# Kernel tuning notes

Measured on AMD Instinct MI355X. Metric: run time of the kernel, lower is better.

Reference implementation:

```python
import jax, jax.numpy as jnp
import numpy as np

B, H, W = 2, 512, 512
EPS = 1e-7


def conv2d(x, w, b, stride=1, pad=1):
    y = jax.lax.conv_general_dilated(x, w, (stride, stride), [(pad, pad), (pad, pad)],
                                     dimension_numbers=('NCHW', 'OIHW', 'NCHW'))
    return y + b[None, :, None, None]


def prelu(x, a):
    return jnp.where(x >= 0, x, a * x)


def feature_ext(x, ws, bs, aa):
    # three-level pyramid: 32ch@full, 64ch@1/2, 96ch@1/4
    x = prelu(conv2d(x, ws[0], bs[0]), aa[0])
    fea1 = prelu(conv2d(x, ws[1], bs[1]), aa[1])
    x = prelu(conv2d(fea1, ws[2], bs[2], stride=2), aa[2])
    fea2 = prelu(conv2d(x, ws[3], bs[3]), aa[3])
    x = prelu(conv2d(fea2, ws[4], bs[4], stride=2), aa[4])
    fea3 = prelu(conv2d(x, ws[5], bs[5]), aa[5])
    return fea1, fea2, fea3


def backwarp(x, flow):
    # grid_sample(bilinear, padding_mode='border', align_corners=True) with pixel-space flow
    b, c, h, w = x.shape
    gy, gx = jnp.meshgrid(jnp.arange(h, dtype=x.dtype), jnp.arange(w, dtype=x.dtype), indexing='ij')
    px = jnp.clip(gx[None] + flow[:, 0], 0.0, w - 1.0)  # (B,h,w)
    py = jnp.clip(gy[None] + flow[:, 1], 0.0, h - 1.0)
    x0f = jnp.floor(px); y0f = jnp.floor(py)
    wx = px - x0f; wy = py - y0f
    x0 = x0f.astype(jnp.int32); y0 = y0f.astype(jnp.int32)
    x1 = jnp.minimum(x0 + 1, w - 1); y1 = jnp.minimum(y0 + 1, h - 1)
    xf = x.reshape(b, c, h * w)

    def gather(ix, iy):
        idx = (iy * w + ix).reshape(b, -1)
        return jax.vmap(lambda v, i: v[:, i])(xf, idx).reshape(b, c, h, w)

    return (gather(x0, y0) * ((1 - wx) * (1 - wy))[:, None]
            + gather(x1, y0) * (wx * (1 - wy))[:, None]
            + gather(x0, y1) * ((1 - wx) * wy)[:, None]
            + gather(x1, y1) * (wx * wy)[:, None])


def softsplat(ten, flow, z):
    # softmax splatting: scatter-add of exp(z)-weighted values + exp(z) normalizer
    b, c, h, w = ten.shape
    ez = jnp.exp(z)                                      # (B,1,h,w)
    vals = jnp.concatenate([ten * ez, ez], axis=1)       # (B,C+1,h,w)
    gy, gx = jnp.meshgrid(jnp.arange(h, dtype=ten.dtype), jnp.arange(w, dtype=ten.dtype), indexing='ij')
    fx = gx[None] + flow[:, 0]
    fy = gy[None] + flow[:, 1]
    x0f = jnp.floor(fx); y0f = jnp.floor(fy)
    x0 = x0f.astype(jnp.int32); y0 = y0f.astype(jnp.int32)
    x1 = x0 + 1; y1 = y0 + 1
    wx1 = fx - x0f; wy1 = fy - y0f
    wx0 = 1.0 - wx1; wy0 = 1.0 - wy1
    corners = [(x0, y0, wx0 * wy0), (x1, y0, wx1 * wy0), (x0, y1, wx0 * wy1), (x1, y1, wx1 * wy1)]
    idxs, wts = [], []
    for cx, cy, cw in corners:
        valid = (cx >= 0) & (cx < w) & (cy >= 0) & (cy < h)
        idxs.append(jnp.where(valid, cy * w + cx, 0).reshape(b, -1))
        wts.append(jnp.where(valid, cw, 0.0).reshape(b, -1))
    idx = jnp.stack(idxs, 1)  # (B,4,HW)
    wt = jnp.stack(wts, 1)
    vflat = vals.reshape(b, c + 1, h * w)

    def scat(v, i, ww):  # v (C+1,HW), i (4,HW), ww (4,HW)
        contrib = (v[:, None, :] * ww[None]).reshape(c + 1, -1)
        return jnp.zeros((c + 1, h * w), v.dtype).at[:, i.reshape(-1)].add(contrib)

    out = jax.vmap(scat)(vflat, idx, wt).reshape(b, c + 1, h, w)
    return out[:, :c] / (out[:, c:] + EPS)


def resize_bl(x, out_h, out_w):
    # bilinear resize, align_corners=False (half-pixel), matches torch interpolate on downsample
    b, c, h, w = x.shape

    def coords(n_out, n_in):
        pos = jnp.clip((jnp.arange(n_out, dtype=x.dtype) + 0.5) * (n_in / n_out) - 0.5, 0.0, n_in - 1.0)
        p0 = jnp.floor(pos)
        i0 = p0.astype(jnp.int32)
        i1 = jnp.minimum(i0 + 1, n_in - 1)
        return i0, i1, pos - p0

    iy0, iy1, wy = coords(out_h, h)
    ix0, ix1, wx = coords(out_w, w)
    x = x[:, :, iy0] * (1 - wy)[None, None, :, None] + x[:, :, iy1] * wy[None, None, :, None]
    x = x[:, :, :, ix0] * (1 - wx) + x[:, :, :, ix1] * wx
    return x


def _forward(input_0, input_1, target_t, flows01, flows10, ws, bs, aa, param_scale):
    fea0 = feature_ext(input_0, ws, bs, aa)
    fea1 = feature_ext(input_1, ws, bs, aa)
    t = target_t[:, None, None, None]

    def splat_map(i0, i1, flows, feas, tt):
        p0 = i0 * 2 - 1
        p1 = i1 * 2 - 1
        err = jnp.mean(jnp.abs(p0 - backwarp(p1, flows[0])), axis=1, keepdims=True)
        z = param_scale * jax.lax.stop_gradient(err)
        imgs, feats = [], []
        for s in range(3):
            f = tt * flows[s]
            hh, ww = H >> s, W >> s
            img = i0 if s == 0 else resize_bl(i0, hh, ww)
            zz = z if s == 0 else resize_bl(z, hh, ww)
            flow_t0 = softsplat(-f, f, zz)
            imgs.append(backwarp(img, flow_t0))
            feats.append(backwarp(feas[s], flow_t0))
        return imgs, feats

    wi0, wf0 = splat_map(input_0, input_1, flows01, fea0, t)
    wi1, wf1 = splat_map(input_1, input_0, flows10, fea1, 1.0 - t)
    level0 = jnp.concatenate([wi0[0], wf0[0], wi1[0], wf1[0]], axis=1)  # (B,70,H,W)
    level1 = jnp.concatenate([wf0[1], wf1[1]], axis=1)                  # (B,128,H/2,W/2)
    level2 = jnp.concatenate([wf0[2], wf1[2]], axis=1)                  # (B,192,H/4,W/4)
    return level0, level1, level2


def setup_inputs() -> dict:
    key = jax.random.key(0)
    ks = jax.random.split(key, 24)
    d = {}
    d['input_0'] = jax.random.uniform(ks[0], (B, 3, H, W), jnp.float32)
    d['input_1'] = jax.random.uniform(ks[1], (B, 3, H, W), jnp.float32)
    d['target_t'] = jax.random.uniform(ks[2], (B,), jnp.float32)
    for i, (nm, s) in enumerate([('flow01_0', 0), ('flow01_1', 1), ('flow01_2', 2),
                                 ('flow10_0', 0), ('flow10_1', 1), ('flow10_2', 2)]):
        d[nm] = jax.random.normal(ks[3 + i], (B, 2, H >> s, W >> s), jnp.float32) * (8.0 / (2 ** s))
    shapes = [(32, 3), (32, 32), (64, 32), (64, 64), (96, 64), (96, 96)]
    for i, (o, c) in enumerate(shapes):
        d['w%d' % (i + 1)] = jax.random.normal(ks[9 + i], (o, c, 3, 3), jnp.float32) * 0.05
        d['b%d' % (i + 1)] = jnp.zeros((o,), jnp.float32)
    d['prelu_a'] = jnp.full((6,), 0.25, jnp.float32)
    d['param_scale'] = jnp.full((1, 1, 1, 1), -1.0, jnp.float32)
    return d


def reference(input_0, input_1, target_t, flow01_0, flow01_1, flow01_2,
              flow10_0, flow10_1, flow10_2,
              w1, b1, w2, b2, w3, b3, w4, b4, w5, b5, w6, b6, prelu_a, param_scale):
    ws = [w1, w2, w3, w4, w5, w6]
    bs = [b1, b2, b3, b4, b5, b6]
    aa = [prelu_a[i] for i in range(6)]
    return _forward(input_0, input_1, target_t,
                    [flow01_0, flow01_1, flow01_2],
                    [flow10_0, flow10_1, flow10_2], ws, bs, aa, param_scale)
```

## Files before the change

kernel.cpp:

```cpp
#include <hip/hip_runtime.h>
#include <math.h>

#define EPSF 1e-7f
constexpr int BB = 2, HH = 512, WWC = 512;

typedef __attribute__((ext_vector_type(4))) float f32x4;
typedef __attribute__((ext_vector_type(8))) _Float16 half8;

struct HZ {
    _Float16* p;
    int Hp, Wp, C;
};
struct HZ5 {
    HZ e[5];
};
__global__ void halo_zero_kernel(HZ5 z) {
    HZ d = z.e[blockIdx.y];
    const int wc = d.Wp * d.C;
    const int side = (d.Hp - 2) * d.C;
    const int perB = 2 * wc + 2 * side;
    const int total = 4 * perB;
    for (int i = blockIdx.x * 256 + threadIdx.x; i < total;
         i += gridDim.x * 256) {
        int b = i / perB, r = i % perB;
        int y, x, c;
        if (r < wc) {
            y = 0; x = r / d.C; c = r % d.C;
        } else if (r < 2 * wc) {
            int q = r - wc;
            y = d.Hp - 1; x = q / d.C; c = q % d.C;
        } else {
            int q = r - 2 * wc;
            int sd = q / side, q2 = q % side;
            y = 1 + q2 / d.C; x = sd ? d.Wp - 1 : 0; c = q2 % d.C;
        }
        d.p[(((size_t)b * d.Hp + y) * d.Wp + x) * d.C + c] = (_Float16)0.f;
    }
}

struct WL {
    const float* w;
    _Float16* dst;
    int IC, OC;
};
struct WL5 {
    WL e[5];
};
__global__ void weight_swz_kernel(WL5 wl) {
    WL d = wl.e[blockIdx.y];
    const int IC = d.IC;
    const int K9 = 9 * IC;
    const int NKC = K9 / 32;
    const int total = d.OC * K9;
    for (int i = blockIdx.x * 256 + threadIdx.x; i < total;
         i += gridDim.x * 256) {
        int j = i & 7;
        int lane = (i >> 3) & 63;
        int rest = i >> 9;
        int kc = rest % NKC;
        int fo = rest / NKC;
        int f = fo & 1, ocblk = fo >> 1;
        int l15 = lane & 15, g = lane >> 4;
        int k = kc * 32 + g * 8 + j;
        int pos = k / IC, ic = k % IC;
        int oc = ocblk * 32 + f * 16 + l15;
        d.dst[i] = (_Float16)d.w[((size_t)oc * IC + ic) * 9 + pos];
    }
}

template <int OCT, int YT>
__global__ __launch_bounds__(256) void conv3x3_nhwc(
    const float* __restrict__ in0, const float* __restrict__ in1,
    const float* __restrict__ wgt, const float* __restrict__ bias,
    const float* __restrict__ prelu_a, int aidx, _Float16* __restrict__ out,
    int IC, int OC, int IH, int IW, int OWp) {
    const int OH = IH, OW = IW;
    extern __shared__ float wsh[];
    const int oc0 = blockIdx.z * OCT;
    const int nw = OCT * IC * 9;
    const float* wsrc = wgt + (size_t)oc0 * IC * 9;
    for (int i = threadIdx.y * 64 + threadIdx.x; i < nw; i += 256)
        wsh[i] = wsrc[i];
    __syncthreads();

    const int ox = blockIdx.x * 64 + threadIdx.x;
    const int BROWS = 4 * YT;
    const int tiles_y = OH / BROWS;
    const int oy0 = (blockIdx.y % tiles_y) * BROWS + threadIdx.y * YT;
    const int b = blockIdx.y / tiles_y;

    float acc[OCT][YT];
#pragma unroll
    for (int j = 0; j < OCT; j++) {
        float bj = bias[oc0 + j];
#pragma unroll
        for (int yy = 0; yy < YT; yy++) acc[j][yy] = bj;
    }

    constexpr int R = YT + 2;
    const float* inb = (b < 2 ? in0 : in1) + (size_t)(b & 1) * IC * IH * IW;
    const int iy0 = oy0 - 1, ix0 = ox - 1;

    for (int ic = 0; ic < IC; ic++) {
        const float* ip = inb + (size_t)ic * IH * IW;
        float v[R][3];
#pragma unroll
        for (int r = 0; r < R; r++) {
            const int iy = iy0 + r;
            const bool yok = (unsigned)iy < (unsigned)IH;
            const float* rp = ip + iy * IW;
#pragma unroll
            for (int c = 0; c < 3; c++) {
                const int ix = ix0 + c;
                v[r][c] = (yok && (unsigned)ix < (unsigned)IW) ? rp[ix] : 0.f;
            }
        }
#pragma unroll
        for (int j = 0; j < OCT; j++) {
            const float* wj = wsh + (j * IC + ic) * 9;
            float w[9];
#pragma unroll
            for (int k = 0; k < 9; k++) w[k] = wj[k];
#pragma unroll
            for (int yy = 0; yy < YT; yy++) {
                float a = acc[j][yy];
#pragma unroll
                for (int ky = 0; ky < 3; ky++)
#pragma unroll
                    for (int kx = 0; kx < 3; kx++)
                        a = fmaf(v[yy + ky][kx], w[ky * 3 + kx], a);
                acc[j][yy] = a;
            }
        }
    }
    const float al = prelu_a[aidx];
    const int OHp = OH + 2;
#pragma unroll
    for (int yy = 0; yy < YT; yy++) {
        _Float16* ob =
            out + (((size_t)b * OHp + (oy0 + yy + 1)) * OWp + (ox + 1)) * OC;
#pragma unroll
        for (int j = 0; j < OCT; j++) {
            float y = acc[j][yy];
            y = y >= 0.f ? y : al * y;
            ob[oc0 + j] = (_Float16)y;
        }
    }
}

template <int S, int IC, int ROWS>
__global__ __launch_bounds__(256) void conv_mfma2(
    const _Float16* __restrict__ in, const _Float16* __restrict__ wswz,
    const float* __restrict__ bias, const float* __restrict__ prelu_a,
    int aidx, _Float16* __restrict__ out, int OC, int IWp, int OH, int OW,
    int OWp) {
    constexpr int NICC = IC / 32;
    constexpr int NKC = 9 * NICC;
    constexpr int NSTG = 2 * NKC * 512;
    extern __shared__ _Float16 bsh[];
    const int oc0 = blockIdx.z * 32;
    {
        const _Float16* src = wswz + (size_t)blockIdx.z * NSTG;
        for (int i = threadIdx.x * 8; i < NSTG; i += 256 * 8)
            *(half8*)(bsh + i) = *(const half8*)(src + i);
    }
    __syncthreads();

    const int lane = threadIdx.x & 63, w = threadIdx.x >> 6;
    const int l15 = lane & 15, g = lane >> 4;
    const int ny = OH / ROWS;
    const int oy0 = (blockIdx.y % ny) * ROWS;
    const int b = blockIdx.y / ny;
    const int xb = blockIdx.x * 128 + w * 32;
    const int IHp = OH * S + 2;
    const _Float16* inb = in + (size_t)b * IHp * IWp * IC;
    const float bv0 = bias[oc0 + l15], bv1 = bias[oc0 + 16 + l15];
    const float al = prelu_a[aidx];
    const size_t aoff0 = (size_t)(xb + l15) * S * IC + g * 8;
    const size_t aoff1 = aoff0 + (size_t)16 * S * IC;
    _Float16* outb = out + (size_t)b * (OH + 2) * OWp * OC;

    for (int ry = 0; ry < ROWS; ++ry) {
        const int oy = oy0 + ry;
        f32x4 acc00 = {bv0, bv0, bv0, bv0}, acc01 = {bv1, bv1, bv1, bv1};
        f32x4 acc10 = {bv0, bv0, bv0, bv0}, acc11 = {bv1, bv1, bv1, bv1};
#pragma unroll
        for (int pos = 0; pos < 9; ++pos) {
            const int ky = pos / 3, kx = pos % 3;
            const _Float16* ap =
                inb + ((size_t)(oy * S + ky) * IWp + kx) * IC;
#pragma unroll
            for (int icc = 0; icc < NICC; ++icc) {
                const int kc = pos * NICC + icc;
                half8 a0 = *(const half8*)(ap + aoff0 + icc * 32);
                half8 a1 = *(const half8*)(ap + aoff1 + icc * 32);
                half8 b0 = *(const half8*)(bsh + kc * 512 + lane * 8);
                half8 b1 = *(const half8*)(bsh + (NKC + kc) * 512 + lane * 8);
                acc00 = __builtin_amdgcn_mfma_f32_16x16x32_f16(a0, b0, acc00,
                                                               0, 0, 0);
                acc01 = __builtin_amdgcn_mfma_f32_16x16x32_f16(a0, b1, acc01,
                                                               0, 0, 0);
                acc10 = __builtin_amdgcn_mfma_f32_16x16x32_f16(a1, b0, acc10,
                                                               0, 0, 0);
                acc11 = __builtin_amdgcn_mfma_f32_16x16x32_f16(a1, b1, acc11,
                                                               0, 0, 0);
            }
        }
#define STORE_FRAG(A, M, N)                                                   \
    {                                                                         \
        _Pragma("unroll") for (int r = 0; r < 4; ++r) {                       \
            int x = xb + (M)*16 + g * 4 + r;                                  \
            float v = (A)[r];                                                 \
            v = v >= 0.f ? v : al * v;                                        \
            outb[((size_t)(oy + 1) * OWp + (x + 1)) * OC + oc0 + (N)*16 +     \
                 l15] = (_Float16)v;                                          \
        }                                                                     \
    }
        STORE_FRAG(acc00, 0, 0)
        STORE_FRAG(acc01, 0, 1)
        STORE_FRAG(acc10, 1, 0)
        STORE_FRAG(acc11, 1, 1)
#undef STORE_FRAG
    }
}

__global__ void compute_z2_kernel(const float* __restrict__ in0,
                                  const float* __restrict__ in1,
                                  const float* __restrict__ f01,
                                  const float* __restrict__ f10,
                                  const float* __restrict__ pscale,
                                  float* __restrict__ z0,
                                  float* __restrict__ z1) {
    int idx = blockIdx.x * blockDim.x + threadIdx.x;
    const int n = BB * HH * WWC;
    if (idx >= n) return;
    const int dir = blockIdx.y;
    const float* i0 = dir ? in1 : in0;
    const float* i1 = dir ? in0 : in1;
    const float* flow = dir ? f10 : f01;
    float* z = dir ? z1 : z0;
    int x = idx % WWC, y = (idx / WWC) % HH, b = idx / (WWC * HH);
    const float* fb = flow + (size_t)b * 2 * HH * WWC;
    float fx = fb[y * WWC + x];
    float fy = fb[HH * WWC + y * WWC + x];
    float px = fminf(fmaxf(x + fx, 0.f), WWC - 1.f);
    float py = fminf(fmaxf(y + fy, 0.f), HH - 1.f);
    float x0f = floorf(px), y0f = floorf(py);
    int x0 = (int)x0f, y0 = (int)y0f;
    int x1 = min(x0 + 1, WWC - 1), y1 = min(y0 + 1, HH - 1);
    float wx = px - x0f, wy = py - y0f;
    float w00 = (1.f - wx) * (1.f - wy), w10 = wx * (1.f - wy);
    float w01 = (1.f - wx) * wy, w11 = wx * wy;
    const float* ib0 = i0 + (size_t)b * 3 * HH * WWC;
    const float* ib1 = i1 + (size_t)b * 3 * HH * WWC;
    float err = 0.f;
#pragma unroll
    for (int c = 0; c < 3; c++) {
        const float* sp = ib1 + (size_t)c * HH * WWC;
        float wv = sp[y0 * WWC + x0] * w00 + sp[y0 * WWC + x1] * w10 +
                   sp[y1 * WWC + x0] * w01 + sp[y1 * WWC + x1] * w11;
        float p0 = 2.f * ib0[(size_t)c * HH * WWC + y * WWC + x] - 1.f;
        err += fabsf(p0 - (2.f * wv - 1.f));
    }
    z[idx] = pscale[0] * (err * (1.f / 3.f));
}

__device__ inline void atomic_add_f32(float* p, float v) {
    __hip_atomic_fetch_add(p, v, __ATOMIC_RELAXED, __HIP_MEMORY_SCOPE_AGENT);
}

__device__ inline float z_sample(const float* __restrict__ zb, int b, int sx,
                                 int sy, int s) {
    const float* zp = zb + (size_t)b * HH * WWC;
    if (s == 0) return zp[sy * WWC + sx];
    float sc = (float)(1 << s);
    float px = fminf(fmaxf((sx + 0.5f) * sc - 0.5f, 0.f), WWC - 1.f);
    float py = fminf(fmaxf((sy + 0.5f) * sc - 0.5f, 0.f), HH - 1.f);
    float x0f = floorf(px), y0f = floorf(py);
    int x0 = (int)x0f, y0 = (int)y0f;
    int x1 = min(x0 + 1, WWC - 1), y1 = min(y0 + 1, HH - 1);
    float wx = px - x0f, wy = py - y0f;
    return zp[y0 * WWC + x0] * (1.f - wx) * (1.f - wy) +
           zp[y0 * WWC + x1] * wx * (1.f - wy) +
           zp[y1 * WWC + x0] * (1.f - wx) * wy + zp[y1 * WWC + x1] * wx * wy;
}

__global__ void splat_far_kernel(const float* __restrict__ fl0,
                                 const float* __restrict__ fl1,
                                 const float* __restrict__ z0,
                                 const float* __restrict__ z1,
                                 const float* __restrict__ tptr,
                                 float* __restrict__ acc, int s, int hh,
                                 int ww) {
    int idx = blockIdx.x * blockDim.x + threadIdx.x;
    const int n = BB * hh * ww;
    if (idx >= n) return;
    const int dir = blockIdx.y;
    const float* flow = dir ? fl1 : fl0;
    const float* z = dir ? z1 : z0;
    float* accd = acc + (size_t)dir * BB * 3 * hh * ww;
    int x = idx % ww, y = (idx / ww) % hh, b = idx / (ww * hh);
    float tt = tptr[b];
    if (dir) tt = 1.f - tt;
    const float* fb = flow + (size_t)b * 2 * hh * ww;
    float fx = tt * fb[y * ww + x];
    float fy = tt * fb[hh * ww + y * ww + x];
    if (fmaxf(fabsf(fx), fabsf(fy)) <= 15.f) return;
    float zz = z_sample(z, b, x, y, s);
    float ez = expf(zz);
    float vx = -fx * ez, vy = -fy * ez;
    float tx = x + fx, ty = y + fy;
    float x0f = floorf(tx), y0f = floorf(ty);
    int x0 = (int)x0f, y0 = (int)y0f;
    int x1 = x0 + 1, y1 = y0 + 1;
    float wx1 = tx - x0f, wy1 = ty - y0f;
    float wx0 = 1.f - wx1, wy0 = 1.f - wy1;
    float* ab = accd + (size_t)b * 3 * hh * ww;
    int cxs[4] = {x0, x1, x0, x1};
    int cys[4] = {y0, y0, y1, y1};
    float cws[4] = {wx0 * wy0, wx1 * wy0, wx0 * wy1, wx1 * wy1};
#pragma unroll
    for (int k = 0; k < 4; k++) {
        int cx = cxs[k], cy = cys[k];
        float w = cws[k];
        if (cx >= 0 && cx < ww && cy >= 0 && cy < hh && w != 0.f) {
            float* p = ab + (size_t)3 * (cy * ww + cx);
            atomic_add_f32(p, vx * w);
            atomic_add_f32(p + 1, vy * w);
            atomic_add_f32(p + 2, ez * w);
        }
    }
}

template <int TH, int TW>
__global__ __launch_bounds__(256) void splat_gather_kernel(
    const float* __restrict__ fl0, const float* __restrict__ fl1,
    const float* __restrict__ z0, const float* __restrict__ z1,
    const float* __restrict__ tptr, float* __restrict__ acc, int s, int hh,
    int ww) {
    constexpr int HALO = 16;
    constexpr int RH = TH + 2 * HALO, RW = TW + 2 * HALO;
    __shared__ float lacc[TH * TW * 3];
    const int x0 = blockIdx.x * TW, y0 = blockIdx.y * TH;
    const int comp = blockIdx.z;
    const int b = comp & (BB - 1), dir = comp / BB;
    const float* flow = dir ? fl1 : fl0;
    const float* z = dir ? z1 : z0;
    float* accd = acc + (size_t)dir * BB * 3 * hh * ww;
    const int tid = threadIdx.x;
    for (int i = tid; i < TH * TW * 3; i += 256) lacc[i] = 0.f;
    __syncthreads();
    float tt = tptr[b];
    if (dir) tt = 1.f - tt;
    const float* fb = flow + (size_t)b * 2 * hh * ww;
    for (int i = tid; i < RH * RW; i += 256) {
        int sy = y0 - HALO + i / RW;
        int sx = x0 - HALO + i % RW;
        if ((unsigned)sy >= (unsigned)hh || (unsigned)sx >= (unsigned)ww)
            continue;
        float fx = tt * fb[sy * ww + sx];
        float fy = tt * fb[(size_t)hh * ww + sy * ww + sx];
        if (fmaxf(fabsf(fx), fabsf(fy)) > 15.f) continue;
        float zz = z_sample(z, b, sx, sy, s);
        float ez = expf(zz);
        float vx = -fx * ez, vy = -fy * ez;
        float tx = sx + fx, ty = sy + fy;
        float xf = floorf(tx), yf = floorf(ty);
        int cx0 = (int)xf - x0, cy0 = (int)yf - y0;
        float wx1 = tx - xf, wy1 = ty - yf;
        float wx0 = 1.f - wx1, wy0 = 1.f - wy1;
#pragma unroll
        for (int k = 0; k < 4; k++) {
            int cx = cx0 + (k & 1), cy = cy0 + (k >> 1);
            float wgt = ((k & 1) ? wx1 : wx0) * ((k >> 1) ? wy1 : wy0);
            if ((unsigned)cx < (unsigned)TW && (unsigned)cy < (unsigned)TH &&
                wgt != 0.f) {
                float* p = lacc + (cy * TW + cx) * 3;
                atomicAdd(p, vx * wgt);
                atomicAdd(p + 1, vy * wgt);
                atomicAdd(p + 2, ez * wgt);
            }
        }
    }
    __syncthreads();
    float* ab = accd + (((size_t)b * hh + y0) * ww + x0) * 3;
    for (int i = tid; i < TH * TW * 3; i += 256) {
        int row = i / (TW * 3), rem = i % (TW * 3);
        float* gp = ab + (size_t)row * ww * 3 + rem;
        *gp = *gp + lacc[i];
    }
}

__global__ void backwarp_s0_kernel(const float* __restrict__ acc,
                                   const float* __restrict__ in0,
                                   const float* __restrict__ in1,
                                   const _Float16* __restrict__ f1,
                                   float* __restrict__ out) {
    int idx = blockIdx.x * blockDim.x + threadIdx.x;
    const int plane = HH * WWC;
    const int n = BB * plane;
    if (idx >= n) return;
    const int dir = blockIdx.y;
    int x = idx % WWC, y = (idx / WWC) % HH, b = idx / plane;
    const float* accd = acc + (size_t)dir * BB * 3 * plane;
    int o = y * WWC + x;
    const float* ap = accd + ((size_t)b * plane + o) * 3;
    float den = ap[2] + EPSF;
    float fx = ap[0] / den;
    float fy = ap[1] / den;
    float px = fminf(fmaxf(x + fx, 0.f), WWC - 1.f);
    float py = fminf(fmaxf(y + fy, 0.f), HH - 1.f);
    float x0f = floorf(px), y0f = floorf(py);
    int x0 = (int)x0f, y0 = (int)y0f;
    int x1 = min(x0 + 1, WWC - 1), y1 = min(y0 + 1, HH - 1);
    float wx = px - x0f, wy = py - y0f;
    float w00 = (1.f - wx) * (1.f - wy), w10 = wx * (1.f - wy);
    float w01 = (1.f - wx) * wy, w11 = wx * wy;
    float* ob = out + (((size_t)b * 70 + dir * 35) * (size_t)plane) + o;
    {
        const float* sb = (dir ? in1 : in0) + (size_t)b * 3 * plane;
        int i00 = y0 * WWC + x0, i10 = y0 * WWC + x1, i01 = y1 * WWC + x0,
            i11 = y1 * WWC + x1;
#pragma unroll
        for (int c = 0; c < 3; c++) {
            const float* sp = sb + (size_t)c * plane;
            float v = sp[i00] * w00 + sp[i10] * w10 + sp[i01] * w01 +
                      sp[i11] * w11;
            ob[(size_t)c * plane] = v;
        }
    }
    {
        const int Wp = WWC + 2, C = 32;
        const _Float16* sb = f1 + (size_t)(dir * 2 + b) * (HH + 2) * Wp * C;
        const _Float16* s00 = sb + ((size_t)(y0 + 1) * Wp + x0 + 1) * C;
        const _Float16* s10 = sb + ((size_t)(y0 + 1) * Wp + x1 + 1) * C;
        const _Float16* s01 = sb + ((size_t)(y1 + 1) * Wp + x0 + 1) * C;
        const _Float16* s11 = sb + ((size_t)(y1 + 1) * Wp + x1 + 1) * C;
        float* obf = ob + (size_t)3 * plane;
        for (int c8 = 0; c8 < C; c8 += 8) {
            half8 v00 = *(const half8*)(s00 + c8);
            half8 v10 = *(const half8*)(s10 + c8);
            half8 v01 = *(const half8*)(s01 + c8);
            half8 v11 = *(const half8*)(s11 + c8);
#pragma unroll
            for (int k = 0; k < 8; k++) {
                float v = (float)v00[k] * w00 + (float)v10[k] * w10 +
                          (float)v01[k] * w01 + (float)v11[k] * w11;
                obf[(size_t)(c8 + k) * plane] = v;
            }
        }
    }
}

__global__ void backwarp_feat_kernel(const float* __restrict__ acc,
                                     const _Float16* __restrict__ src,
                                     float* __restrict__ out, int C, int hh,
                                     int ww, int Wp) {
    int idx = blockIdx.x * blockDim.x + threadIdx.x;
    const int n = BB * hh * ww;
    if (idx >= n) return;
    const int dir = blockIdx.y;
    int x = idx % ww, y = (idx / ww) % hh, b = idx / (ww * hh);
    const int plane = hh * ww;
    const float* accd = acc + (size_t)dir * BB * 3 * plane;
    const float* ap = accd + ((size_t)b * plane + y * ww + x) * 3;
    float den = ap[2] + EPSF;
    float fx = ap[0] / den;
    float fy = ap[1] / den;
    float px = fminf(fmaxf(x + fx, 0.f), ww - 1.f);
    float py = fminf(fmaxf(y + fy, 0.f), hh - 1.f);
    float x0f = floorf(px), y0f = floorf(py);
    int x0 = (int)x0f, y0 = (int)y0f;
    int x1 = min(x0 + 1, ww - 1), y1 = min(y0 + 1, hh - 1);
    float wx = px - x0f, wy = py - y0f;
    float w00 = (1.f - wx) * (1.f - wy), w10 = wx * (1.f - wy);
    float w01 = (1.f - wx) * wy, w11 = wx * wy;
    const int Hp = hh + 2;
    const _Float16* sb = src + (size_t)(dir * 2 + b) * Hp * Wp * C;
    const _Float16* s00 = sb + ((size_t)(y0 + 1) * Wp + x0 + 1) * C;
    const _Float16* s10 = sb + ((size_t)(y0 + 1) * Wp + x1 + 1) * C;
    const _Float16* s01 = sb + ((size_t)(y1 + 1) * Wp + x0 + 1) * C;
    const _Float16* s11 = sb + ((size_t)(y1 + 1) * Wp + x1 + 1) * C;
    float* ob = out + (((size_t)b * 2 * C + dir * C) * (size_t)plane) +
                y * ww + x;
    for (int c8 = 0; c8 < C; c8 += 8) {
        half8 v00 = *(const half8*)(s00 + c8);
        half8 v10 = *(const half8*)(s10 + c8);
        half8 v01 = *(const half8*)(s01 + c8);
        half8 v11 = *(const half8*)(s11 + c8);
#pragma unroll
        for (int k = 0; k < 8; k++) {
            float v = (float)v00[k] * w00 + (float)v10[k] * w10 +
                      (float)v01[k] * w01 + (float)v11[k] * w11;
            ob[(size_t)(c8 + k) * plane] = v;
        }
    }
}

extern "C" void kernel_launch(void* const* d_in, const int* in_sizes, int n_in,
                              void* d_out, int out_size, void* d_ws,
                              size_t ws_size, hipStream_t stream) {
    const float* input0 = (const float*)d_in[0];
    const float* input1 = (const float*)d_in[1];
    const float* tgt = (const float*)d_in[2];
    const float* flows[2][3] = {
        {(const float*)d_in[3], (const float*)d_in[4], (const float*)d_in[5]},
        {(const float*)d_in[6], (const float*)d_in[7], (const float*)d_in[8]}};
    const float* w[6];
    const float* bs[6];
    for (int i = 0; i < 6; i++) {
        w[i] = (const float*)d_in[9 + 2 * i];
        bs[i] = (const float*)d_in[10 + 2 * i];
    }
    const float* prelu_a = (const float*)d_in[21];
    const float* pscale = (const float*)d_in[22];
    float* out = (float*)d_out;

    _Float16* hb = (_Float16*)d_ws;
    const size_t A1 = (size_t)4 * 514 * 514 * 32;
    const size_t A2 = (size_t)4 * 258 * 258 * 64;
    const size_t A3 = (size_t)4 * 130 * 130 * 96;
    _Float16* act1 = hb;
    _Float16* f1 = act1 + A1;
    _Float16* act2 = f1 + A1;
    _Float16* f2 = act2 + A2;
    _Float16* act3 = f2 + A2;
    _Float16* f3 = act3 + A3;
    float* fb32 = (float*)(f3 + A3);
    float* zb0 = fb32;
    float* zb1 = zb0 + (size_t)BB * HH * WWC;
    float* acc = zb1 + (size_t)BB * HH * WWC;
    _Float16* wswz = (_Float16*)(acc + (size_t)2 * BB * 3 * HH * WWC);
    const size_t WO2 = 0, WO3 = 9216, WO4 = 27648, WO5 = 64512, WO6 = 119808;

    {
        WL5 wlist;
        wlist.e[0] = {w[1], wswz + WO2, 32, 32};
        wlist.e[1] = {w[2], wswz + WO3, 32, 64};
        wlist.e[2] = {w[3], wswz + WO4, 64, 64};
        wlist.e[3] = {w[4], wswz + WO5, 64, 96};
        wlist.e[4] = {w[5], wswz + WO6, 96, 96};
        dim3 grd(16, 5);
        weight_swz_kernel<<<grd, 256, 0, stream>>>(wlist);
    }
    {
        HZ5 hz;
        hz.e[0] = {act1, 514, 514, 32};
        hz.e[1] = {f1, 514, 514, 32};
        hz.e[2] = {act2, 258, 258, 64};
        hz.e[3] = {f2, 258, 258, 64};
        hz.e[4] = {act3, 130, 130, 96};
        dim3 grd(32, 5);
        halo_zero_kernel<<<grd, 256, 0, stream>>>(hz);
    }

    {
        dim3 blk(64, 4);
        dim3 grd(512 / 64, (512 / 16) * 4, 32 / 16);
        size_t sm = (size_t)16 * 3 * 9 * sizeof(float);
        conv3x3_nhwc<16, 4><<<grd, blk, sm, stream>>>(
            input0, input1, w[0], bs[0], prelu_a, 0, act1, 3, 32, 512, 512,
            514);
    }
    {
        dim3 grd(512 / 128, (512 / 4) * 4, 1);
        conv_mfma2<1, 32, 4><<<grd, 256, 18432, stream>>>(
            act1, wswz + WO2, bs[1], prelu_a, 1, f1, 32, 514, 512, 512, 514);
    }
    {
        dim3 grd(256 / 128, (256 / 4) * 4, 2);
        conv_mfma2<2, 32, 4><<<grd, 256, 18432, stream>>>(
            f1, wswz + WO3, bs[2], prelu_a, 2, act2, 64, 514, 256, 256, 258);
    }
    {
        dim3 grd(256 / 128, (256 / 4) * 4, 2);
        conv_mfma2<1, 64, 4><<<grd, 256, 36864, stream>>>(
            act2, wswz + WO4, bs[3], prelu_a, 3, f2, 64, 258, 256, 256, 258);
    }
    {
        dim3 grd(1, (128 / 2) * 4, 3);
        conv_mfma2<2, 64, 2><<<grd, 256, 36864, stream>>>(
            f2, wswz + WO5, bs[4], prelu_a, 4, act3, 96, 258, 128, 128, 130);
    }
    {
        dim3 grd(1, (128 / 2) * 4, 3);
        conv_mfma2<1, 96, 2><<<grd, 256, 55296, stream>>>(
            act3, wswz + WO6, bs[5], prelu_a, 5, f3, 96, 130, 128, 128, 130);
    }

    {
        int n = BB * HH * WWC;
        dim3 grd((n + 255) / 256, 2);
        compute_z2_kernel<<<grd, 256, 0, stream>>>(
            input0, input1, flows[0][0], flows[1][0], pscale, zb0, zb1);
    }

    const size_t l1off = (size_t)BB * 70 * 512 * 512;
    const size_t l2off = l1off + (size_t)BB * 128 * 256 * 256;

    for (int s = 0; s < 3; s++) {
        int hh = HH >> s, ww = WWC >> s;
        int n = BB * hh * ww;
        hipMemsetAsync(acc, 0, (size_t)2 * BB * 3 * hh * ww * sizeof(float),
                       stream);
        {
            dim3 grd((n + 255) / 256, 2);
            splat_far_kernel<<<grd, 256, 0, stream>>>(
                flows[0][s], flows[1][s], zb0, zb1, tgt, acc, s, hh, ww);
        }
        if (s < 2) {
            dim3 grd(ww / 64, hh / 32, 2 * BB);
            splat_gather_kernel<32, 64><<<grd, 256, 0, stream>>>(
                flows[0][s], flows[1][s], zb0, zb1, tgt, acc, s, hh, ww);
        } else {
            dim3 grd(ww / 32, hh / 16, 2 * BB);
            splat_gather_kernel<16, 32><<<grd, 256, 0, stream>>>(
                flows[0][s], flows[1][s], zb0, zb1, tgt, acc, s, hh, ww);
        }
        dim3 grd((n + 255) / 256, 2);
        if (s == 0) {
            backwarp_s0_kernel<<<grd, 256, 0, stream>>>(acc, input0, input1,
                                                        f1, out);
        } else if (s == 1) {
            backwarp_feat_kernel<<<grd, 256, 0, stream>>>(
                acc, f2, out + l1off, 64, 256, 256, 258);
        } else {
            backwarp_feat_kernel<<<grd, 256, 0, stream>>>(
                acc, f3, out + l2off, 96, 128, 128, 130);
        }
    }
}
```

Before: 1.000 ms.

## Restructure MFMA conv to compute all output channels per wave, read weights from global

The MFMA conv kernel is rewritten so each wave computes a 64-pixel strip across all output channels (4 M-fragments by OC/16 N-fragments) instead of 32 pixels by 32 channels. Input activations are then loaded once per pixel for every output channel rather than once per 32-channel block. Weight staging through shared memory is removed, and B fragments are read directly from global memory, relying on cache. The weight swizzle layout is flattened to match. The cost is more accumulator registers per thread, possibly lower occupancy, and weight reads that no longer come from LDS.

```diff
diff --git a/kernel.cpp b/kernel.cpp
--- a/kernel.cpp
+++ b/kernel.cpp
@@ -58,12 +58,11 @@
         int lane = (i >> 3) & 63;
         int rest = i >> 9;
         int kc = rest % NKC;
-        int fo = rest / NKC;
-        int f = fo & 1, ocblk = fo >> 1;
+        int N = rest / NKC;
         int l15 = lane & 15, g = lane >> 4;
         int k = kc * 32 + g * 8 + j;
         int pos = k / IC, ic = k % IC;
-        int oc = ocblk * 32 + f * 16 + l15;
+        int oc = N * 16 + l15;
         d.dst[i] = (_Float16)d.w[((size_t)oc * IC + ic) * 9 + pos];
     }
 }
@@ -148,80 +147,74 @@
     }
 }
 
-template <int S, int IC, int ROWS>
-__global__ __launch_bounds__(256) void conv_mfma2(
+template <int S, int IC, int OC, int WPR>
+__global__ __launch_bounds__(256) void conv_mfma3(
     const _Float16* __restrict__ in, const _Float16* __restrict__ wswz,
     const float* __restrict__ bias, const float* __restrict__ prelu_a,
-    int aidx, _Float16* __restrict__ out, int OC, int IWp, int OH, int OW,
-    int OWp) {
+    int aidx, _Float16* __restrict__ out, int IWp, int OH, int OW, int OWp) {
     constexpr int NICC = IC / 32;
     constexpr int NKC = 9 * NICC;
-    constexpr int NSTG = 2 * NKC * 512;
-    extern __shared__ _Float16 bsh[];
-    const int oc0 = blockIdx.z * 32;
-    {
-        const _Float16* src = wswz + (size_t)blockIdx.z * NSTG;
-        for (int i = threadIdx.x * 8; i < NSTG; i += 256 * 8)
-            *(half8*)(bsh + i) = *(const half8*)(src + i);
-    }
-    __syncthreads();
-
+    constexpr int NFR = OC / 16;
+    constexpr int RPB = 4 / WPR;
     const int lane = threadIdx.x & 63, w = threadIdx.x >> 6;
     const int l15 = lane & 15, g = lane >> 4;
-    const int ny = OH / ROWS;
-    const int oy0 = (blockIdx.y % ny) * ROWS;
+    const int ny = OH / RPB;
+    const int oy = (blockIdx.y % ny) * RPB + w / WPR;
     const int b = blockIdx.y / ny;
-    const int xb = blockIdx.x * 128 + w * 32;
+    const int xb = blockIdx.x * (WPR * 64) + (w % WPR) * 64;
     const int IHp = OH * S + 2;
     const _Float16* inb = in + (size_t)b * IHp * IWp * IC;
-    const float bv0 = bias[oc0 + l15], bv1 = bias[oc0 + 16 + l15];
     const float al = prelu_a[aidx];
-    const size_t aoff0 = (size_t)(xb + l15) * S * IC + g * 8;
-    const size_t aoff1 = aoff0 + (size_t)16 * S * IC;
+
+    f32x4 acc[4][NFR];
+#pragma unroll
+    for (int n = 0; n < NFR; ++n) {
+        float bv = bias[n * 16 + l15];
+#pragma unroll
+        for (int m = 0; m < 4; ++m) acc[m][n] = {bv, bv, bv, bv};
+    }
+    size_t aoff[4];
+#pragma unroll
+    for (int m = 0; m < 4; ++m)
+        aoff[m] = (size_t)(xb + m * 16 + l15) * S * IC + g * 8;
+    const int boff = lane * 8;
+
+#pragma unroll
+    for (int pos = 0; pos < 9; ++pos) {
+        const int ky = pos / 3, kx = pos % 3;
+        const _Float16* ap = inb + ((size_t)(oy * S + ky) * IWp + kx) * IC;
+#pragma unroll
+        for (int icc = 0; icc < NICC; ++icc) {
+            const int kc = pos * NICC + icc;
+            half8 a[4];
+#pragma unroll
+            for (int m = 0; m < 4; ++m)
+                a[m] = *(const half8*)(ap + aoff[m] + icc * 32);
+#pragma unroll
+            for (int n = 0; n < NFR; ++n) {
+                half8 bf = *(const half8*)(wswz +
+                                           (size_t)(n * NKC + kc) * 512 +
+                                           boff);
+#pragma unroll
+                for (int m = 0; m < 4; ++m)
+                    acc[m][n] = __builtin_amdgcn_mfma_f32_16x16x32_f16(
+                        a[m], bf, acc[m][n], 0, 0, 0);
+            }
+        }
+    }
     _Float16* outb = out + (size_t)b * (OH + 2) * OWp * OC;
-
-    for (int ry = 0; ry < ROWS; ++ry) {
-        const int oy = oy0 + ry;
-        f32x4 acc00 = {bv0, bv0, bv0, bv0}, acc01 = {bv1, bv1, bv1, bv1};
-        f32x4 acc10 = {bv0, bv0, bv0, bv0}, acc11 = {bv1, bv1, bv1, bv1};
-#pragma unroll
-        for (int pos = 0; pos < 9; ++pos) {
-            const int ky = pos / 3, kx = pos % 3;
-            const _Float16* ap =
-                inb + ((size_t)(oy * S + ky) * IWp + kx) * IC;
-#pragma unroll
-            for (int icc = 0; icc < NICC; ++icc) {
-                const int kc = pos * NICC + icc;
-                half8 a0 = *(const half8*)(ap + aoff0 + icc * 32);
-                half8 a1 = *(const half8*)(ap + aoff1 + icc * 32);
-                half8 b0 = *(const half8*)(bsh + kc * 512 + lane * 8);
-                half8 b1 = *(const half8*)(bsh + (NKC + kc) * 512 + lane * 8);
-                acc00 = __builtin_amdgcn_mfma_f32_16x16x32_f16(a0, b0, acc00,
-                                                               0, 0, 0);
-                acc01 = __builtin_amdgcn_mfma_f32_16x16x32_f16(a0, b1, acc01,
-                                                               0, 0, 0);
-                acc10 = __builtin_amdgcn_mfma_f32_16x16x32_f16(a1, b0, acc10,
-                                                               0, 0, 0);
-                acc11 = __builtin_amdgcn_mfma_f32_16x16x32_f16(a1, b1, acc11,
-                                                               0, 0, 0);
+#pragma unroll
+    for (int m = 0; m < 4; ++m)
+#pragma unroll
+        for (int n = 0; n < NFR; ++n)
+#pragma unroll
+            for (int r = 0; r < 4; ++r) {
+                int x = xb + m * 16 + g * 4 + r;
+                float v = acc[m][n][r];
+                v = v >= 0.f ? v : al * v;
+                outb[((size_t)(oy + 1) * OWp + (x + 1)) * OC + n * 16 + l15] =
+                    (_Float16)v;
             }
-        }
-#define STORE_FRAG(A, M, N)                                                   \
-    {                                                                         \
-        _Pragma("unroll") for (int r = 0; r < 4; ++r) {                       \
-            int x = xb + (M)*16 + g * 4 + r;                                  \
-            float v = (A)[r];                                                 \
-            v = v >= 0.f ? v : al * v;                                        \
-            outb[((size_t)(oy + 1) * OWp + (x + 1)) * OC + oc0 + (N)*16 +     \
-                 l15] = (_Float16)v;                                          \
-        }                                                                     \
-    }
-        STORE_FRAG(acc00, 0, 0)
-        STORE_FRAG(acc01, 0, 1)
-        STORE_FRAG(acc10, 1, 0)
-        STORE_FRAG(acc11, 1, 1)
-#undef STORE_FRAG
-    }
 }
 
 __global__ void compute_z2_kernel(const float* __restrict__ in0,
@@ -563,29 +556,29 @@
             514);
     }
     {
-        dim3 grd(512 / 128, (512 / 4) * 4, 1);
-        conv_mfma2<1, 32, 4><<<grd, 256, 18432, stream>>>(
-            act1, wswz + WO2, bs[1], prelu_a, 1, f1, 32, 514, 512, 512, 514);
-    }
-    {
-        dim3 grd(256 / 128, (256 / 4) * 4, 2);
-        conv_mfma2<2, 32, 4><<<grd, 256, 18432, stream>>>(
-            f1, wswz + WO3, bs[2], prelu_a, 2, act2, 64, 514, 256, 256, 258);
-    }
-    {
-        dim3 grd(256 / 128, (256 / 4) * 4, 2);
-        conv_mfma2<1, 64, 4><<<grd, 256, 36864, stream>>>(
-            act2, wswz + WO4, bs[3], prelu_a, 3, f2, 64, 258, 256, 256, 258);
-    }
-    {
-        dim3 grd(1, (128 / 2) * 4, 3);
-        conv_mfma2<2, 64, 2><<<grd, 256, 36864, stream>>>(
-            f2, wswz + WO5, bs[4], prelu_a, 4, act3, 96, 258, 128, 128, 130);
-    }
-    {
-        dim3 grd(1, (128 / 2) * 4, 3);
-        conv_mfma2<1, 96, 2><<<grd, 256, 55296, stream>>>(
-            act3, wswz + WO6, bs[5], prelu_a, 5, f3, 96, 130, 128, 128, 130);
+        dim3 grd(512 / 256, 512 * 4, 1);
+        conv_mfma3<1, 32, 32, 4><<<grd, 256, 0, stream>>>(
+            act1, wswz + WO2, bs[1], prelu_a, 1, f1, 514, 512, 512, 514);
+    }
+    {
+        dim3 grd(1, 256 * 4, 1);
+        conv_mfma3<2, 32, 64, 4><<<grd, 256, 0, stream>>>(
+            f1, wswz + WO3, bs[2], prelu_a, 2, act2, 514, 256, 256, 258);
+    }
+    {
+        dim3 grd(1, 256 * 4, 1);
+        conv_mfma3<1, 64, 64, 4><<<grd, 256, 0, stream>>>(
+            act2, wswz + WO4, bs[3], prelu_a, 3, f2, 258, 256, 256, 258);
+    }
+    {
+        dim3 grd(1, (128 / 2) * 4, 1);
+        conv_mfma3<2, 64, 96, 2><<<grd, 256, 0, stream>>>(
+            f2, wswz + WO5, bs[4], prelu_a, 4, act3, 258, 128, 128, 130);
+    }
+    {
+        dim3 grd(1, (128 / 2) * 4, 1);
+        conv_mfma3<1, 96, 96, 2><<<grd, 256, 0, stream>>>(
+            act3, wswz + WO6, bs[5], prelu_a, 5, f3, 130, 128, 128, 130);
     }
 
     {
```

Result: faster. 943.1 us (-5.7%).
